# Kernel tuning notes

Measured on AMD Instinct MI355X. Metric: run time of the kernel, lower is better.

Reference implementation:

```python
import jax, jax.numpy as jnp
import numpy as np

MARGIN = 70.0
THR = 125.0
PD_EPS = 1e-6  # torch F.pairwise_distance default eps


def _return_cam(features, weight_softmax, class_idx):
    # features: [bz, nc, h, w]; weight_softmax: [n_cls, nc]; class_idx: [bz]
    w_sel = weight_softmax[class_idx]                     # [bz, nc]
    cam = jnp.einsum('bc,bchw->bhw', w_sel, features)     # [bz, h, w]
    cam = cam - cam.min(axis=(1, 2), keepdims=True)
    cam = cam / cam.max(axis=(1, 2), keepdims=True) * 255.0
    return cam[:, None]                                   # [bz, 1, h, w]


def _pairwise_distance(x, y):
    # torch F.pairwise_distance: ||x - y + eps||_2 along last dim
    return jnp.sqrt(jnp.sum((x - y + PD_EPS) ** 2, axis=-1))


def setup_inputs() -> dict:
    key = jax.random.key(0)
    ks = jax.random.split(key, 6)
    bz, nc, h, w, n_cls = 64, 2048, 14, 14, 1000
    return {
        'pred': jax.random.normal(ks[0], (bz, n_cls), jnp.float32),
        'cla_truth': jax.random.randint(ks[1], (bz,), 0, n_cls, jnp.int32),
        'seg_truth': jax.random.uniform(ks[2], (bz, h, w), jnp.float32),
        'features_blobs': jax.random.normal(ks[3], (bz, nc, h, w), jnp.float32),
        'weight_softmax': jax.random.normal(ks[4], (n_cls, nc), jnp.float32),
        'idx': jax.random.randint(ks[5], (bz, 3), 0, n_cls, jnp.int32),
    }


def reference(pred, cla_truth, seg_truth, features_blobs, weight_softmax, idx):
    bz, nc, h, w = features_blobs.shape
    # cross entropy
    logp = jax.nn.log_softmax(pred, axis=-1)
    loss1 = -jnp.mean(logp[jnp.arange(bz), cla_truth])
    # CAMs for top-3 predicted classes
    cam0 = _return_cam(features_blobs, weight_softmax, idx[:, 0])  # [bz,1,h,w]
    cam1 = _return_cam(features_blobs, weight_softmax, idx[:, 1])
    cam2 = _return_cam(features_blobs, weight_softmax, idx[:, 2])
    # binarize cam0 (values in [0,255]); <=thr -> 0, >thr -> 1
    dst = jnp.where(cam0[:, 0] > THR, 1.0, 0.0)                     # [bz,h,w]
    # row-wise distance to seg truth, averaged over rows
    ed1 = jnp.mean(_pairwise_distance(dst, seg_truth), axis=1)      # [bz]
    # CAM-weighted features via broadcasted matmul (requires h == w)
    fea0 = jnp.matmul(cam0, features_blobs)                         # [bz,nc,h,w]
    fea1 = jnp.matmul(cam1, features_blobs)
    fea2 = jnp.matmul(cam2, features_blobs)
    d01 = _pairwise_distance(fea0.reshape(bz, -1), fea1.reshape(bz, -1)) / nc
    d02 = _pairwise_distance(fea0.reshape(bz, -1), fea2.reshape(bz, -1)) / nc
    loss_dis = jnp.mean(ed1 + jnp.clip(MARGIN - d01 - d02, 0.0, None)) + loss1
    return loss_dis
```

## Files before the change

### kernel.cpp

```cpp
#include <hip/hip_runtime.h>
#include <math.h>

#define BZ      64
#define NC      2048
#define HH      14
#define HW      196
#define NCLS    1000
#define SPLITS  8
#define CPB     (NC/SPLITS)
#define CHUNK   8
#define NCHUNK  (CPB/CHUNK)
#define LPAD    200
#define NTRI    105

#define CAM_OFF  0
#define G_OFF    (BZ*SPLITS*3*HW)
#define S_OFF    (G_OFF + BZ*SPLITS*HW)
#define CE_OFF   (S_OFF + BZ*SPLITS*HH)
#define TICK_OFF (CE_OFF + BZ)

template<int MODE>
__device__ __forceinline__ float bred(float v, float* red){
  #pragma unroll
  for (int o=32;o>0;o>>=1){
    float u = __shfl_down(v, o, 64);
    if (MODE==0) v += u; else if (MODE==1) v = fminf(v,u); else v = fmaxf(v,u);
  }
  __syncthreads();
  if ((threadIdx.x & 63)==0) red[threadIdx.x>>6] = v;
  __syncthreads();
  float r = red[0];
  #pragma unroll
  for (int w=1;w<4;w++){
    float u = red[w];
    if (MODE==0) r += u; else if (MODE==1) r = fminf(r,u); else r = fmaxf(r,u);
  }
  return r;
}

__global__ __launch_bounds__(256) void k_init(
    const float* __restrict__ pred, const int* __restrict__ cla,
    float* __restrict__ ws)
{
  const int t = threadIdx.x, b = blockIdx.x;
  __shared__ float red[4];
  if (t == 0) ((int*)ws)[TICK_OFF + b] = 0;

  const float* pb = pred + (size_t)b*NCLS;
  float mv = -3.0e38f;
  for (int i=t;i<NCLS;i+=256) mv = fmaxf(mv, pb[i]);
  mv = bred<2>(mv, red);
  float es = 0.f;
  for (int i=t;i<NCLS;i+=256) es += expf(pb[i]-mv);
  es = bred<0>(es, red);
  if (t==0){
    float lse = mv + logf(es);
    ws[CE_OFF + b] = lse - pb[cla[b]];
  }
}

__global__ __launch_bounds__(256) void k_main(
    const float* __restrict__ F, const float* __restrict__ W,
    const int* __restrict__ idx, const float* __restrict__ seg,
    float* __restrict__ ws, float* __restrict__ out)
{
  __shared__ __align__(16) float Fs[2][CHUNK*LPAD];
  __shared__ __align__(16) float wls[3][CPB];
  __shared__ __align__(16) float sred[HW];
  __shared__ int lastFlag;
  __shared__ __align__(16) union Ovl {
    float gacc[112*NTRI];
    struct {
      float cam[3][HW]; float Gt[NTRI]; float Sv[HH];
      float D1[HW]; float D2[HW]; float EE[HW];
      float rowv[HH]; float dc1[HH]; float dc2[HH];
      float red[4]; float scal[6];
    } p2;
  } U;

  const int t = threadIdx.x;
  const int s = blockIdx.x;
  const int b = blockIdx.y;
  const int cbase = s*CPB;

  {
    const int i0 = idx[b*3+0], i1 = idx[b*3+1], i2 = idx[b*3+2];
    wls[0][t] = W[(size_t)i0*NC + cbase + t];
    wls[1][t] = W[(size_t)i1*NC + cbase + t];
    wls[2][t] = W[(size_t)i2*NC + cbase + t];

    const float4* Fb4 = (const float4*)(F + ((size_t)b*NC + cbase)*HW);

    const bool isG   = (t < 112);
    const int  cL    = t & 7;
    const int  jc    = t >> 3;
    const bool isCam = (t >= 128 && t < 177);
    const int  cp    = t - 128;
    const bool isLd  = (t < 196);

    float acc[NTRI];
    #pragma unroll
    for (int k=0;k<NTRI;k++) acc[k]=0.f;
    float4 c0a = make_float4(0.f,0.f,0.f,0.f);
    float4 c1a = make_float4(0.f,0.f,0.f,0.f);
    float4 c2a = make_float4(0.f,0.f,0.f,0.f);
    float4 sA  = make_float4(0.f,0.f,0.f,0.f);

    float4 p0, p1;
    auto loadChunk = [&](int ch){
      if (isLd){
        const float4* src = Fb4 + (size_t)ch*392;
        p0 = src[2*t]; p1 = src[2*t+1];
      }
    };
    auto storeChunk = [&](int bufi){
      if (isLd){
        float4* dst = (float4*)(&Fs[bufi][0]);
        int i = 2*t;   dst[(i/49)*(LPAD/4) + (i%49)] = p0;
        i = 2*t+1;     dst[(i/49)*(LPAD/4) + (i%49)] = p1;
      }
    };

    loadChunk(0);
    storeChunk(0);
    __syncthreads();

    #pragma unroll 1
    for (int ch = 0; ch < NCHUNK; ++ch){
      const int bufi = ch & 1;
      if (ch+1 < NCHUNK) loadChunk(ch+1);
      const float* Fsb = &Fs[bufi][0];

      if (isG){
        const float* colp = Fsb + cL*LPAD + jc;
        float x[14];
        #pragma unroll
        for (int m=0;m<14;m++) x[m] = colp[m*HH];
        #pragma unroll
        for (int m=0;m<14;m++){
          #pragma unroll
          for (int n=m;n<14;n++){
            acc[14*m - (m*(m-1))/2 + (n-m)] += x[m]*x[n];
          }
        }
      }
      if (isCam){
        float w0a[CHUNK], w1a[CHUNK], w2a[CHUNK];
        *(float4*)&w0a[0] = *(const float4*)&wls[0][ch*CHUNK];
        *(float4*)&w0a[4] = *(const float4*)&wls[0][ch*CHUNK+4];
        *(float4*)&w1a[0] = *(const float4*)&wls[1][ch*CHUNK];
        *(float4*)&w1a[4] = *(const float4*)&wls[1][ch*CHUNK+4];
        *(float4*)&w2a[0] = *(const float4*)&wls[2][ch*CHUNK];
        *(float4*)&w2a[4] = *(const float4*)&wls[2][ch*CHUNK+4];
        #pragma unroll
        for (int c=0;c<CHUNK;c++){
          float4 v = *(const float4*)(Fsb + c*LPAD + 4*cp);
          c0a.x += w0a[c]*v.x; c0a.y += w0a[c]*v.y; c0a.z += w0a[c]*v.z; c0a.w += w0a[c]*v.w;
          c1a.x += w1a[c]*v.x; c1a.y += w1a[c]*v.y; c1a.z += w1a[c]*v.z; c1a.w += w1a[c]*v.w;
          c2a.x += w2a[c]*v.x; c2a.y += w2a[c]*v.y; c2a.z += w2a[c]*v.z; c2a.w += w2a[c]*v.w;
          sA.x += v.x; sA.y += v.y; sA.z += v.z; sA.w += v.w;
        }
      }
      if (ch+1 < NCHUNK) storeChunk((ch+1)&1);
      __syncthreads();
    }

    const size_t pslot = (size_t)(b*SPLITS + s);
    if (isCam){
      float* base = ws + CAM_OFF + pslot*3*HW;
      *(float4*)(base          + 4*cp) = c0a;
      *(float4*)(base + HW     + 4*cp) = c1a;
      *(float4*)(base + 2*HW   + 4*cp) = c2a;
      *(float4*)(sred + 4*cp) = sA;
    }
    if (isG){
      float* gr = &U.gacc[t*NTRI];
      #pragma unroll
      for (int k=0;k<NTRI;k++) gr[k] = acc[k];
    }
    __syncthreads();

    if (t < NTRI){
      float a = 0.f;
      for (int th=0; th<112; th++) a += U.gacc[th*NTRI + t];
      ws[G_OFF + pslot*HW + t] = a;
    }
    if (t >= 128 && t < 128+HH){
      int r = t - 128;
      float a = 0.f;
      #pragma unroll
      for (int j=0;j<HH;j++) a += sred[r*HH+j];
      ws[S_OFF + pslot*HH + r] = a;
    }
    __syncthreads();
  }

  if (t == 0){
    __threadfence();
    int old = atomicAdd(&((int*)ws)[TICK_OFF + b], 1);
    lastFlag = (old == SPLITS-1) ? 1 : 0;
    __threadfence();
  }
  __syncthreads();

  if (lastFlag){
    volatile const float* vws = (volatile const float*)ws;

    if (t < HW){
      for (int k=0;k<3;k++){
        float a=0.f;
        for (int sp=0;sp<SPLITS;sp++)
          a += vws[CAM_OFF + ((size_t)(b*SPLITS+sp)*3 + k)*HW + t];
        U.p2.cam[k][t]=a;
      }
    }
    if (t < NTRI){
      float g=0.f;
      for (int sp=0;sp<SPLITS;sp++) g += vws[G_OFF + (size_t)(b*SPLITS+sp)*HW + t];
      U.p2.Gt[t]=g;
    }
    if (t < HH){
      float a=0.f;
      for (int sp=0;sp<SPLITS;sp++) a += vws[S_OFF + (size_t)(b*SPLITS+sp)*HH + t];
      U.p2.Sv[t]=a;
    }
    __syncthreads();

    for (int k=0;k<3;k++){
      float v = (t<HW)? U.p2.cam[k][t] : 3.0e38f;
      float mn = bred<1>(v, U.p2.red);
      v = (t<HW)? U.p2.cam[k][t] : -3.0e38f;
      float mx = bred<2>(v, U.p2.red);
      if (t==0){ U.p2.scal[2*k]=mn; U.p2.scal[2*k+1]=mx; }
    }
    __syncthreads();

    if (t < HW){
      float c0 = (U.p2.cam[0][t]-U.p2.scal[0]) / (U.p2.scal[1]-U.p2.scal[0]) * 255.0f;
      float c1 = (U.p2.cam[1][t]-U.p2.scal[2]) / (U.p2.scal[3]-U.p2.scal[2]) * 255.0f;
      float c2 = (U.p2.cam[2][t]-U.p2.scal[4]) / (U.p2.scal[5]-U.p2.scal[4]) * 255.0f;
      float dst = (c0 > 125.0f) ? 1.0f : 0.0f;
      U.p2.D1[t] = c0 - c1; U.p2.D2[t] = c0 - c2;
      float e = dst - seg[(size_t)b*HW + t] + 1e-6f;
      U.p2.EE[t] = e*e;
    }
    __syncthreads();

    if (t < HH){
      float rs=0.f, d1=0.f, d2=0.f;
      #pragma unroll
      for (int j=0;j<HH;j++){
        rs += U.p2.EE[t*HH+j];
        d1 += U.p2.D1[j*HH+t];
        d2 += U.p2.D2[j*HH+t];
      }
      U.p2.rowv[t] = sqrtf(rs); U.p2.dc1[t]=d1; U.p2.dc2[t]=d2;
    }
    __syncthreads();

    float v1=0.f, v2=0.f;
    if (t < HW){
      int m = t/HH, mp = t%HH;
      float h1=0.f, h2=0.f;
      #pragma unroll
      for (int i=0;i<HH;i++){
        h1 += U.p2.D1[i*HH+m]*U.p2.D1[i*HH+mp];
        h2 += U.p2.D2[i*HH+m]*U.p2.D2[i*HH+mp];
      }
      int mm = (m<mp)?m:mp, nn = (m<mp)?mp:m;
      float g = U.p2.Gt[14*mm - (mm*(mm-1))/2 + (nn-mm)];
      v1 = h1*g; v2 = h2*g;
    }
    float sx2_1 = bred<0>(v1, U.p2.red);
    float sx2_2 = bred<0>(v2, U.p2.red);

    if (t==0){
      float ce = vws[CE_OFF + b];
      float ed1 = 0.f;
      #pragma unroll
      for (int i=0;i<HH;i++) ed1 += U.p2.rowv[i];
      ed1 *= (1.0f/14.0f);
      float sx1=0.f, sx2=0.f;
      #pragma unroll
      for (int m=0;m<HH;m++){ sx1 += U.p2.dc1[m]*U.p2.Sv[m]; sx2 += U.p2.dc2[m]*U.p2.Sv[m]; }
      const float NEPS2 = 401408.0f * 1e-12f;
      float d01 = sqrtf(sx2_1 + 2e-6f*sx1 + NEPS2) * (1.0f/2048.0f);
      float d02 = sqrtf(sx2_2 + 2e-6f*sx2 + NEPS2) * (1.0f/2048.0f);
      float term = ed1 + fmaxf(0.0f, 70.0f - d01 - d02) + ce;
      atomicAdd(out, term * (1.0f/64.0f));
    }
  }
}

extern "C" void kernel_launch(void* const* d_in, const int* in_sizes, int n_in,
                              void* d_out, int out_size, void* d_ws, size_t ws_size,
                              hipStream_t stream) {
  const float* pred = (const float*)d_in[0];
  const int*   cla  = (const int*)  d_in[1];
  const float* seg  = (const float*)d_in[2];
  const float* F    = (const float*)d_in[3];
  const float* W    = (const float*)d_in[4];
  const int*   idx  = (const int*)  d_in[5];
  float* out = (float*)d_out;
  float* ws  = (float*)d_ws;

  k_init<<<BZ, 256, 0, stream>>>(pred, cla, ws);
  k_main<<<dim3(SPLITS, BZ), 256, 0, stream>>>(F, W, idx, seg, ws, out);
}
```

Baseline: 208.0 us.

## Split Gram accumulation across two thread teams and spread CAM work per pixel

The 105 Gram-matrix accumulators are divided between two 112-thread teams, each holding about 53 accumulators. This lowers per-thread register pressure, and launch bounds now request two blocks per CU. CAM and column-sum work moves from 49 threads handling float4 to 196 threads handling one pixel each, so the work spreads across more waves. The cost is that each team re-reads the 14 column values, and the shared reduction buffer grows slightly.

```diff
diff --git a/kernel.cpp b/kernel.cpp
--- a/kernel.cpp
+++ b/kernel.cpp
@@ -12,6 +12,7 @@
 #define NCHUNK  (CPB/CHUNK)
 #define LPAD    200
 #define NTRI    105
+#define KSPL    53
 
 #define CAM_OFF  0
 #define G_OFF    (BZ*SPLITS*3*HW)
@@ -36,6 +37,22 @@
     if (MODE==0) r += u; else if (MODE==1) r = fminf(r,u); else r = fmaxf(r,u);
   }
   return r;
+}
+
+template<int LO, int HI>
+__device__ __forceinline__ void gramStep(const float* __restrict__ colp,
+                                         float* __restrict__ acc){
+  float x[14];
+  #pragma unroll
+  for (int m=0;m<14;m++) x[m] = colp[m*HH];
+  #pragma unroll
+  for (int m=0;m<14;m++){
+    #pragma unroll
+    for (int n=m;n<14;n++){
+      const int k = 14*m - (m*(m-1))/2 + (n-m);
+      if (k >= LO && k < HI) acc[k-LO] += x[m]*x[n];
+    }
+  }
 }
 
 __global__ __launch_bounds__(256) void k_init(
@@ -59,7 +76,7 @@
   }
 }
 
-__global__ __launch_bounds__(256) void k_main(
+__global__ __launch_bounds__(256, 2) void k_main(
     const float* __restrict__ F, const float* __restrict__ W,
     const int* __restrict__ idx, const float* __restrict__ seg,
     float* __restrict__ ws, float* __restrict__ out)
@@ -69,7 +86,7 @@
   __shared__ __align__(16) float sred[HW];
   __shared__ int lastFlag;
   __shared__ __align__(16) union Ovl {
-    float gacc[112*NTRI];
+    float gacc[224*KSPL];
     struct {
       float cam[3][HW]; float Gt[NTRI]; float Sv[HH];
       float D1[HW]; float D2[HW]; float EE[HW];
@@ -83,6 +100,13 @@
   const int b = blockIdx.y;
   const int cbase = s*CPB;
 
+  const int gteam = (t < 112) ? 0 : ((t >= 128 && t < 240) ? 1 : -1);
+  const int cc    = (t < 128) ? t : (t - 128);
+  const int cL    = cc & 7;
+  const int jc    = cc >> 3;
+  const bool isCam = (t < 196);
+  const bool isLd  = (t < 196);
+
   {
     const int i0 = idx[b*3+0], i1 = idx[b*3+1], i2 = idx[b*3+2];
     wls[0][t] = W[(size_t)i0*NC + cbase + t];
@@ -91,20 +115,10 @@
 
     const float4* Fb4 = (const float4*)(F + ((size_t)b*NC + cbase)*HW);
 
-    const bool isG   = (t < 112);
-    const int  cL    = t & 7;
-    const int  jc    = t >> 3;
-    const bool isCam = (t >= 128 && t < 177);
-    const int  cp    = t - 128;
-    const bool isLd  = (t < 196);
-
-    float acc[NTRI];
+    float acc[KSPL];
     #pragma unroll
-    for (int k=0;k<NTRI;k++) acc[k]=0.f;
-    float4 c0a = make_float4(0.f,0.f,0.f,0.f);
-    float4 c1a = make_float4(0.f,0.f,0.f,0.f);
-    float4 c2a = make_float4(0.f,0.f,0.f,0.f);
-    float4 sA  = make_float4(0.f,0.f,0.f,0.f);
+    for (int k=0;k<KSPL;k++) acc[k]=0.f;
+    float cam0=0.f, cam1=0.f, cam2=0.f, ssum=0.f;
 
     float4 p0, p1;
     auto loadChunk = [&](int ch){
@@ -131,18 +145,10 @@
       if (ch+1 < NCHUNK) loadChunk(ch+1);
       const float* Fsb = &Fs[bufi][0];
 
-      if (isG){
-        const float* colp = Fsb + cL*LPAD + jc;
-        float x[14];
-        #pragma unroll
-        for (int m=0;m<14;m++) x[m] = colp[m*HH];
-        #pragma unroll
-        for (int m=0;m<14;m++){
-          #pragma unroll
-          for (int n=m;n<14;n++){
-            acc[14*m - (m*(m-1))/2 + (n-m)] += x[m]*x[n];
-          }
-        }
+      if (gteam == 0){
+        gramStep<0,KSPL>(Fsb + cL*LPAD + jc, acc);
+      } else if (gteam == 1){
+        gramStep<KSPL,NTRI>(Fsb + cL*LPAD + jc, acc);
       }
       if (isCam){
         float w0a[CHUNK], w1a[CHUNK], w2a[CHUNK];
@@ -154,11 +160,8 @@
         *(float4*)&w2a[4] = *(const float4*)&wls[2][ch*CHUNK+4];
         #pragma unroll
         for (int c=0;c<CHUNK;c++){
-          float4 v = *(const float4*)(Fsb + c*LPAD + 4*cp);
-          c0a.x += w0a[c]*v.x; c0a.y += w0a[c]*v.y; c0a.z += w0a[c]*v.z; c0a.w += w0a[c]*v.w;
-          c1a.x += w1a[c]*v.x; c1a.y += w1a[c]*v.y; c1a.z += w1a[c]*v.z; c1a.w += w1a[c]*v.w;
-          c2a.x += w2a[c]*v.x; c2a.y += w2a[c]*v.y; c2a.z += w2a[c]*v.z; c2a.w += w2a[c]*v.w;
-          sA.x += v.x; sA.y += v.y; sA.z += v.z; sA.w += v.w;
+          float v = Fsb[c*LPAD + t];
+          cam0 += w0a[c]*v; cam1 += w1a[c]*v; cam2 += w2a[c]*v; ssum += v;
         }
       }
       if (ch+1 < NCHUNK) storeChunk((ch+1)&1);
@@ -168,21 +171,29 @@
     const size_t pslot = (size_t)(b*SPLITS + s);
     if (isCam){
       float* base = ws + CAM_OFF + pslot*3*HW;
-      *(float4*)(base          + 4*cp) = c0a;
-      *(float4*)(base + HW     + 4*cp) = c1a;
-      *(float4*)(base + 2*HW   + 4*cp) = c2a;
-      *(float4*)(sred + 4*cp) = sA;
-    }
-    if (isG){
-      float* gr = &U.gacc[t*NTRI];
-      #pragma unroll
-      for (int k=0;k<NTRI;k++) gr[k] = acc[k];
+      base[t]        = cam0;
+      base[HW + t]   = cam1;
+      base[2*HW + t] = cam2;
+      sred[t] = ssum;
+    }
+    if (gteam == 0){
+      float* gr = &U.gacc[(size_t)cc*KSPL];
+      #pragma unroll
+      for (int k=0;k<KSPL;k++) gr[k] = acc[k];
+    } else if (gteam == 1){
+      float* gr = &U.gacc[(size_t)(112+cc)*KSPL];
+      #pragma unroll
+      for (int k=0;k<NTRI-KSPL;k++) gr[k] = acc[k];
     }
     __syncthreads();
 
     if (t < NTRI){
       float a = 0.f;
-      for (int th=0; th<112; th++) a += U.gacc[th*NTRI + t];
+      if (t < KSPL){
+        for (int r=0; r<112; r++)   a += U.gacc[(size_t)r*KSPL + t];
+      } else {
+        for (int r=112; r<224; r++) a += U.gacc[(size_t)r*KSPL + (t-KSPL)];
+      }
       ws[G_OFF + pslot*HW + t] = a;
     }
     if (t >= 128 && t < 128+HH){
```

New measurement: 207.3 us. About the same (-0.4%).

## Restructure Gram accumulation into 2x2 register tiles and double channel splits

Applied to the files above, without the earlier changes.

Replaces the per-thread 105-entry upper-triangle Gram accumulator with 224 threads, each computing a 2x2 tile over one channel of the chunk. This cuts register pressure and the large shared-memory reduction buffer. Channel splits double from 8 to 16 so more blocks run per batch, and blocks grow to 320 threads with the CAM threads moved to the first wave. The padded smem layout is dropped, which may add bank conflicts, and the larger split count adds partial-sum traffic in the final reduction.

```diff
diff --git a/kernel.cpp b/kernel.cpp
--- a/kernel.cpp
+++ b/kernel.cpp
@@ -6,12 +6,10 @@
 #define HH      14
 #define HW      196
 #define NCLS    1000
-#define SPLITS  8
+#define SPLITS  16
 #define CPB     (NC/SPLITS)
 #define CHUNK   8
 #define NCHUNK  (CPB/CHUNK)
-#define LPAD    200
-#define NTRI    105
 
 #define CAM_OFF  0
 #define G_OFF    (BZ*SPLITS*3*HW)
@@ -19,7 +17,7 @@
 #define CE_OFF   (S_OFF + BZ*SPLITS*HH)
 #define TICK_OFF (CE_OFF + BZ)
 
-template<int MODE>
+template<int MODE, int NW>
 __device__ __forceinline__ float bred(float v, float* red){
   #pragma unroll
   for (int o=32;o>0;o>>=1){
@@ -31,7 +29,7 @@
   __syncthreads();
   float r = red[0];
   #pragma unroll
-  for (int w=1;w<4;w++){
+  for (int w=1;w<NW;w++){
     float u = red[w];
     if (MODE==0) r += u; else if (MODE==1) r = fminf(r,u); else r = fmaxf(r,u);
   }
@@ -49,34 +47,35 @@
   const float* pb = pred + (size_t)b*NCLS;
   float mv = -3.0e38f;
   for (int i=t;i<NCLS;i+=256) mv = fmaxf(mv, pb[i]);
-  mv = bred<2>(mv, red);
+  mv = bred<2,4>(mv, red);
   float es = 0.f;
   for (int i=t;i<NCLS;i+=256) es += expf(pb[i]-mv);
-  es = bred<0>(es, red);
+  es = bred<0,4>(es, red);
   if (t==0){
     float lse = mv + logf(es);
     ws[CE_OFF + b] = lse - pb[cla[b]];
   }
 }
 
-__global__ __launch_bounds__(256) void k_main(
+__global__ __launch_bounds__(320) void k_main(
     const float* __restrict__ F, const float* __restrict__ W,
     const int* __restrict__ idx, const float* __restrict__ seg,
     float* __restrict__ ws, float* __restrict__ out)
 {
-  __shared__ __align__(16) float Fs[2][CHUNK*LPAD];
+  __shared__ __align__(16) union Ovl {
+    float Fs[2][CHUNK*HW];
+    struct {
+      float cam[3][HW]; float Gm[HW]; float Sv[HH];
+      float D1[HW]; float D2[HW]; float EE[HW];
+      float rowv[HH]; float dc1[HH]; float dc2[HH];
+      float scal[6];
+    } p2;
+  } U;
   __shared__ __align__(16) float wls[3][CPB];
   __shared__ __align__(16) float sred[HW];
+  __shared__ __align__(16) float gred[224*4];
+  __shared__ float red[5];
   __shared__ int lastFlag;
-  __shared__ __align__(16) union Ovl {
-    float gacc[112*NTRI];
-    struct {
-      float cam[3][HW]; float Gt[NTRI]; float Sv[HH];
-      float D1[HW]; float D2[HW]; float EE[HW];
-      float rowv[HH]; float dc1[HH]; float dc2[HH];
-      float red[4]; float scal[6];
-    } p2;
-  } U;
 
   const int t = threadIdx.x;
   const int s = blockIdx.x;
@@ -85,39 +84,45 @@
 
   {
     const int i0 = idx[b*3+0], i1 = idx[b*3+1], i2 = idx[b*3+2];
-    wls[0][t] = W[(size_t)i0*NC + cbase + t];
-    wls[1][t] = W[(size_t)i1*NC + cbase + t];
-    wls[2][t] = W[(size_t)i2*NC + cbase + t];
-
-    const float4* Fb4 = (const float4*)(F + ((size_t)b*NC + cbase)*HW);
-
-    const bool isG   = (t < 112);
-    const int  cL    = t & 7;
-    const int  jc    = t >> 3;
-    const bool isCam = (t >= 128 && t < 177);
-    const int  cp    = t - 128;
-    const bool isLd  = (t < 196);
-
-    float acc[NTRI];
-    #pragma unroll
-    for (int k=0;k<NTRI;k++) acc[k]=0.f;
+    if (t < CPB){
+      wls[0][t] = W[(size_t)i0*NC + cbase + t];
+      wls[1][t] = W[(size_t)i1*NC + cbase + t];
+      wls[2][t] = W[(size_t)i2*NC + cbase + t];
+    }
+
+    const float* Fb = F + ((size_t)b*NC + cbase)*HW;
+
+    const bool isCam = (t < 49);
+    const bool isG   = (t >= 64 && t < 288);
+    int m0=0,m1=0,n0=0,n1=0, cg=0;
+    if (isG){
+      int g = t - 64;
+      int tile = g % 28; cg = g / 28;
+      int k = tile, tm = 0;
+      while (k >= 7 - tm){ k -= 7 - tm; tm++; }
+      int tn = tm + k;
+      m0 = 2*tm; m1 = m0+1; n0 = 2*tn; n1 = n0+1;
+    }
+
     float4 c0a = make_float4(0.f,0.f,0.f,0.f);
     float4 c1a = make_float4(0.f,0.f,0.f,0.f);
     float4 c2a = make_float4(0.f,0.f,0.f,0.f);
     float4 sA  = make_float4(0.f,0.f,0.f,0.f);
-
-    float4 p0, p1;
+    float g00=0.f, g01=0.f, g10=0.f, g11=0.f;
+
+    float4 pre0 = make_float4(0.f,0.f,0.f,0.f);
+    float4 pre1 = make_float4(0.f,0.f,0.f,0.f);
+
     auto loadChunk = [&](int ch){
-      if (isLd){
-        const float4* src = Fb4 + (size_t)ch*392;
-        p0 = src[2*t]; p1 = src[2*t+1];
+      if (t < 196){
+        const float4* src = (const float4*)(Fb + (size_t)ch*CHUNK*HW);
+        pre0 = src[2*t]; pre1 = src[2*t+1];
       }
     };
     auto storeChunk = [&](int bufi){
-      if (isLd){
-        float4* dst = (float4*)(&Fs[bufi][0]);
-        int i = 2*t;   dst[(i/49)*(LPAD/4) + (i%49)] = p0;
-        i = 2*t+1;     dst[(i/49)*(LPAD/4) + (i%49)] = p1;
+      if (t < 196){
+        float4* dst = (float4*)(&U.Fs[bufi][0]);
+        dst[2*t] = pre0; dst[2*t+1] = pre1;
       }
     };
 
@@ -129,21 +134,8 @@
     for (int ch = 0; ch < NCHUNK; ++ch){
       const int bufi = ch & 1;
       if (ch+1 < NCHUNK) loadChunk(ch+1);
-      const float* Fsb = &Fs[bufi][0];
-
-      if (isG){
-        const float* colp = Fsb + cL*LPAD + jc;
-        float x[14];
-        #pragma unroll
-        for (int m=0;m<14;m++) x[m] = colp[m*HH];
-        #pragma unroll
-        for (int m=0;m<14;m++){
-          #pragma unroll
-          for (int n=m;n<14;n++){
-            acc[14*m - (m*(m-1))/2 + (n-m)] += x[m]*x[n];
-          }
-        }
-      }
+      const float* Fsb = &U.Fs[bufi][0];
+
       if (isCam){
         float w0a[CHUNK], w1a[CHUNK], w2a[CHUNK];
         *(float4*)&w0a[0] = *(const float4*)&wls[0][ch*CHUNK];
@@ -154,13 +146,28 @@
         *(float4*)&w2a[4] = *(const float4*)&wls[2][ch*CHUNK+4];
         #pragma unroll
         for (int c=0;c<CHUNK;c++){
-          float4 v = *(const float4*)(Fsb + c*LPAD + 4*cp);
+          float4 v = *(const float4*)(Fsb + c*HW + 4*t);
           c0a.x += w0a[c]*v.x; c0a.y += w0a[c]*v.y; c0a.z += w0a[c]*v.z; c0a.w += w0a[c]*v.w;
           c1a.x += w1a[c]*v.x; c1a.y += w1a[c]*v.y; c1a.z += w1a[c]*v.z; c1a.w += w1a[c]*v.w;
           c2a.x += w2a[c]*v.x; c2a.y += w2a[c]*v.y; c2a.z += w2a[c]*v.z; c2a.w += w2a[c]*v.w;
           sA.x += v.x; sA.y += v.y; sA.z += v.z; sA.w += v.w;
         }
       }
+      if (isG){
+        const float* Mb = Fsb + cg*HW;
+        const float2* r0 = (const float2*)(Mb + m0*HH);
+        const float2* r1 = (const float2*)(Mb + m1*HH);
+        const float2* q0 = (const float2*)(Mb + n0*HH);
+        const float2* q1 = (const float2*)(Mb + n1*HH);
+        #pragma unroll
+        for (int jj=0;jj<7;jj++){
+          float2 a0=r0[jj], a1=r1[jj], b0=q0[jj], b1=q1[jj];
+          g00 += a0.x*b0.x + a0.y*b0.y;
+          g01 += a0.x*b1.x + a0.y*b1.y;
+          g10 += a1.x*b0.x + a1.y*b0.y;
+          g11 += a1.x*b1.x + a1.y*b1.y;
+        }
+      }
       if (ch+1 < NCHUNK) storeChunk((ch+1)&1);
       __syncthreads();
     }
@@ -168,29 +175,37 @@
     const size_t pslot = (size_t)(b*SPLITS + s);
     if (isCam){
       float* base = ws + CAM_OFF + pslot*3*HW;
-      *(float4*)(base          + 4*cp) = c0a;
-      *(float4*)(base + HW     + 4*cp) = c1a;
-      *(float4*)(base + 2*HW   + 4*cp) = c2a;
-      *(float4*)(sred + 4*cp) = sA;
+      *(float4*)(base          + 4*t) = c0a;
+      *(float4*)(base + HW     + 4*t) = c1a;
+      *(float4*)(base + 2*HW   + 4*t) = c2a;
+      *(float4*)(sred + 4*t) = sA;
     }
     if (isG){
-      float* gr = &U.gacc[t*NTRI];
-      #pragma unroll
-      for (int k=0;k<NTRI;k++) gr[k] = acc[k];
-    }
-    __syncthreads();
-
-    if (t < NTRI){
-      float a = 0.f;
-      for (int th=0; th<112; th++) a += U.gacc[th*NTRI + t];
-      ws[G_OFF + pslot*HW + t] = a;
-    }
-    if (t >= 128 && t < 128+HH){
-      int r = t - 128;
-      float a = 0.f;
-      #pragma unroll
-      for (int j=0;j<HH;j++) a += sred[r*HH+j];
-      ws[S_OFF + pslot*HH + r] = a;
+      int g = t - 64;
+      float* gr = &gred[g*4];
+      gr[0]=g00; gr[1]=g01; gr[2]=g10; gr[3]=g11;
+    }
+    __syncthreads();
+
+    if (t < HH){
+      float a=0.f;
+      #pragma unroll
+      for (int j=0;j<HH;j++) a += sred[t*HH+j];
+      ws[S_OFF + pslot*HH + t] = a;
+    }
+    if (t < 112){
+      int tile = t >> 2, q = t & 3;
+      int k = tile, tm2 = 0;
+      while (k >= 7 - tm2){ k -= 7 - tm2; tm2++; }
+      int tn2 = tm2 + k;
+      float a=0.f;
+      #pragma unroll
+      for (int c=0;c<8;c++) a += gred[(c*28+tile)*4 + q];
+      int aa = q>>1, bb = q&1;
+      int mm = 2*tm2 + aa, nn = 2*tn2 + bb;
+      float* gb = ws + G_OFF + pslot*HW;
+      gb[mm*HH+nn] = a;
+      if (tn2 > tm2) gb[nn*HH+mm] = a;
     }
     __syncthreads();
   }
@@ -213,11 +228,9 @@
           a += vws[CAM_OFF + ((size_t)(b*SPLITS+sp)*3 + k)*HW + t];
         U.p2.cam[k][t]=a;
       }
-    }
-    if (t < NTRI){
       float g=0.f;
       for (int sp=0;sp<SPLITS;sp++) g += vws[G_OFF + (size_t)(b*SPLITS+sp)*HW + t];
-      U.p2.Gt[t]=g;
+      U.p2.Gm[t]=g;
     }
     if (t < HH){
       float a=0.f;
@@ -228,9 +241,9 @@
 
     for (int k=0;k<3;k++){
       float v = (t<HW)? U.p2.cam[k][t] : 3.0e38f;
-      float mn = bred<1>(v, U.p2.red);
+      float mn = bred<1,5>(v, red);
       v = (t<HW)? U.p2.cam[k][t] : -3.0e38f;
-      float mx = bred<2>(v, U.p2.red);
+      float mx = bred<2,5>(v, red);
       if (t==0){ U.p2.scal[2*k]=mn; U.p2.scal[2*k+1]=mx; }
     }
     __syncthreads();
@@ -267,12 +280,10 @@
         h1 += U.p2.D1[i*HH+m]*U.p2.D1[i*HH+mp];
         h2 += U.p2.D2[i*HH+m]*U.p2.D2[i*HH+mp];
       }
-      int mm = (m<mp)?m:mp, nn = (m<mp)?mp:m;
-      float g = U.p2.Gt[14*mm - (mm*(mm-1))/2 + (nn-mm)];
-      v1 = h1*g; v2 = h2*g;
-    }
-    float sx2_1 = bred<0>(v1, U.p2.red);
-    float sx2_2 = bred<0>(v2, U.p2.red);
+      v1 = h1*U.p2.Gm[t]; v2 = h2*U.p2.Gm[t];
+    }
+    float sx2_1 = bred<0,5>(v1, red);
+    float sx2_2 = bred<0,5>(v2, red);
 
     if (t==0){
       float ce = vws[CE_OFF + b];
@@ -305,5 +316,5 @@
   float* ws  = (float*)d_ws;
 
   k_init<<<BZ, 256, 0, stream>>>(pred, cla, ws);
-  k_main<<<dim3(SPLITS, BZ), 256, 0, stream>>>(F, W, idx, seg, ws, out);
+  k_main<<<dim3(SPLITS, BZ), 320, 0, stream>>>(F, W, idx, seg, ws, out);
 }
```

New measurement: 248.3 us. 1.19x slower.
